# Kernel optimization log

Hardware: AMD Instinct MI355X
Metric: run time of the kernel (lower is better)

The kernel has to match this reference:

```python
import jax, jax.numpy as jnp
import numpy as np

MUL = 64      # multiplicity of each irrep (64x0e + 64x1o)
B = 8192      # batch / number of nodes
INV_SQRT3 = float(1.0 / np.sqrt(3.0))  # e3nn wigner_3j normalization for (1,1,0),(0,1,1),(1,0,1)
# component normalization: alpha = sqrt(dim_out / fan_in), fan_in = sum over paths of mul_u*mul_v
FAN_IN = 2 * MUL * MUL  # two paths feed each output irrep
ALPHA0 = float(np.sqrt(1.0 / FAN_IN))  # l_out = 0, dim 1
ALPHA1 = float(np.sqrt(3.0 / FAN_IN))  # l_out = 1, dim 3


def setup_inputs() -> dict:
    key = jax.random.key(0)
    kx, k0, k1, k2, k3 = jax.random.split(key, 5)
    x = jax.random.normal(kx, (B, 4 * MUL), dtype=jnp.float32)  # [B, 64*1 + 64*3]
    w000 = jax.random.normal(k0, (MUL, MUL, MUL), dtype=jnp.float32)  # 0e x 0e -> 0e
    w110 = jax.random.normal(k1, (MUL, MUL, MUL), dtype=jnp.float32)  # 1o x 1o -> 0e
    w011 = jax.random.normal(k2, (MUL, MUL, MUL), dtype=jnp.float32)  # 0e x 1o -> 1o
    w101 = jax.random.normal(k3, (MUL, MUL, MUL), dtype=jnp.float32)  # 1o x 0e -> 1o
    return {"x": x, "w000": w000, "w110": w110, "w011": w011, "w101": w101}


def reference(x, w000, w110, w011, w101):
    # split concatenated irrep features: scalars then vectors
    x0 = x[:, :MUL]                          # [B, U]      l=0 (e)
    x1 = x[:, MUL:].reshape(-1, MUL, 3)      # [B, U, 3]   l=1 (o)

    # path (0e,0e)->0e : CG = 1
    p000 = jnp.einsum('uvw,bu,bv->bw', w000, x0, x0)
    # path (1o,1o)->0e : CG[i,j] = delta_ij / sqrt(3)
    p110 = jnp.einsum('uvw,bui,bvi->bw', w110, x1, x1) * INV_SQRT3
    out0 = ALPHA0 * (p000 + p110)            # [B, W]

    # path (0e,1o)->1o : CG[j,k] = delta_jk / sqrt(3)
    p011 = jnp.einsum('uvw,bu,bvk->bwk', w011, x0, x1) * INV_SQRT3
    # path (1o,0e)->1o : CG[i,k] = delta_ik / sqrt(3)
    p101 = jnp.einsum('uvw,buk,bv->bwk', w101, x1, x0) * INV_SQRT3
    out1 = ALPHA1 * (p011 + p101)            # [B, W, 3]

    return jnp.concatenate([out0, out1.reshape(out1.shape[0], MUL * 3)], axis=-1)
```

## Files before the change

kernel.cpp:

```cpp
#include <hip/hip_runtime.h>
#include <hip/hip_bf16.h>
#include <cstdint>

#define BM 32
#define NTHREADS 640
#define WS_TILE 524288
#define SMEM_BYTES (4*64*32*4 + 6*32*64*4)

typedef __bf16 bf16x8_t __attribute__((ext_vector_type(8)));
typedef float f32x4_t __attribute__((ext_vector_type(4)));

__global__ __launch_bounds__(256) void prep_weights(const float* __restrict__ w000,
                                                    const float* __restrict__ w110,
                                                    const float* __restrict__ w011,
                                                    const float* __restrict__ w101,
                                                    char* __restrict__ ws) {
  const float A0  = 0.011048543456039806f;
  const float A0I = A0 * 0.57735026918962576f;
  int t = blockIdx.x * 256 + threadIdx.x;
  int u = t >> 9, f = (t >> 6) & 7, l = t & 63;
  int n = f >> 1, kf = f & 1;
  int w = 16 * n + (l & 15);
  int vbase = 8 * (l >> 4) + 32 * kf;
  bf16x8_t p0, p1, pc;
#pragma unroll
  for (int j = 0; j < 8; ++j) {
    int v = vbase + j;
    float a = w000[u * 4096 + v * 64 + w] * A0;
    float b = w110[u * 4096 + v * 64 + w] * A0I;
    float d = (w011[u * 4096 + v * 64 + w] + w101[v * 4096 + u * 64 + w]) * A0;
    p0[j] = (__bf16)a;
    p1[j] = (__bf16)b;
    pc[j] = (__bf16)d;
  }
  int off = u * 8192 + f * 1024 + l * 16;
  *(bf16x8_t*)(ws + off) = p0;
  *(bf16x8_t*)(ws + WS_TILE + off) = p1;
  *(bf16x8_t*)(ws + 2 * WS_TILE + off) = pc;
}

__global__ __launch_bounds__(NTHREADS, 1) void tp_main(const float* __restrict__ x,
                                                       const char* __restrict__ ws,
                                                       float* __restrict__ out) {
  extern __shared__ char smem[];
  float* xS   = (float*)smem;
  float* pscr = (float*)(smem + 32768);
  const int tid = threadIdx.x;
  const int wave = tid >> 6, lane = tid & 63;
  const int lr = lane & 15, lg = lane >> 4;
  const int b0 = blockIdx.x * BM;
  const int unit = wave >> 1;
  const int kf = wave & 1;
  const int tsel = (unit == 0) ? 0 : ((unit == 1) ? 1 : 2);
  const char* gw = ws + tsel * WS_TILE + kf * 1024 + lane * 16;

  for (int idx = tid; idx < 4 * 64 * 32; idx += NTHREADS) {
    int vec = idx >> 11, rem = idx & 2047;
    int uu = rem >> 5, bb = rem & 31;
    int col = (vec == 0) ? uu : (64 + 3 * uu + (vec - 1));
    xS[idx] = x[(b0 + bb) * 256 + col];
  }

  float xp[3][2][8];
  if (unit == 1) {
#pragma unroll
    for (int vi = 0; vi < 3; ++vi)
#pragma unroll
      for (int m = 0; m < 2; ++m)
#pragma unroll
        for (int j = 0; j < 8; ++j) {
          int v = 8 * lg + 32 * kf + j;
          xp[vi][m][j] = x[(b0 + 16 * m + lr) * 256 + 64 + 3 * v + vi];
        }
  } else {
#pragma unroll
    for (int m = 0; m < 2; ++m)
#pragma unroll
      for (int j = 0; j < 8; ++j) {
        int v = 8 * lg + 32 * kf + j;
        int col = (unit == 0) ? v : (64 + 3 * v + (unit - 2));
        xp[0][m][j] = x[(b0 + 16 * m + lr) * 256 + col];
      }
  }

  f32x4_t acc[2][4];
#pragma unroll
  for (int m = 0; m < 2; ++m)
#pragma unroll
    for (int n = 0; n < 4; ++n) {
      f32x4_t z = {0.f, 0.f, 0.f, 0.f};
      acc[m][n] = z;
    }

  auto LOADG = [&](bf16x8_t (&bfr)[4], int uu) {
    const char* p = gw + uu * 8192;
#pragma unroll
    for (int n = 0; n < 4; ++n)
      bfr[n] = *(const bf16x8_t*)(p + n * 2048);
  };

  auto STEP = [&](bf16x8_t (&bfr)[4], int uu) {
    bf16x8_t afr[2];
    if (unit == 1) {
#pragma unroll
      for (int m = 0; m < 2; ++m) {
        float s0 = xS[1 * 2048 + uu * 32 + 16 * m + lr];
        float s1 = xS[2 * 2048 + uu * 32 + 16 * m + lr];
        float s2 = xS[3 * 2048 + uu * 32 + 16 * m + lr];
#pragma unroll
        for (int j = 0; j < 8; ++j)
          afr[m][j] = (__bf16)(s0 * xp[0][m][j] + s1 * xp[1][m][j] + s2 * xp[2][m][j]);
      }
    } else {
#pragma unroll
      for (int m = 0; m < 2; ++m) {
        float s = xS[uu * 32 + 16 * m + lr];
#pragma unroll
        for (int j = 0; j < 8; ++j)
          afr[m][j] = (__bf16)(s * xp[0][m][j]);
      }
    }
#pragma unroll
    for (int m = 0; m < 2; ++m)
#pragma unroll
      for (int n = 0; n < 4; ++n)
        acc[m][n] = __builtin_amdgcn_mfma_f32_16x16x32_bf16(afr[m], bfr[n], acc[m][n], 0, 0, 0);
  };

  __syncthreads();

  bf16x8_t B0[4], B1[4], B2[4];
  LOADG(B0, 0);
  LOADG(B1, 1);
  for (int u = 0; u < 60; u += 3) {
    LOADG(B2, u + 2);
    STEP(B0, u);
    LOADG(B0, u + 3);
    STEP(B1, u + 1);
    LOADG(B1, u + 4);
    STEP(B2, u + 2);
  }
  LOADG(B2, 62);
  STEP(B0, 60);
  LOADG(B0, 63);
  STEP(B1, 61);
  STEP(B2, 62);
  STEP(B0, 63);

  if (kf == 1) {
#pragma unroll
    for (int m = 0; m < 2; ++m)
#pragma unroll
      for (int n = 0; n < 4; ++n)
#pragma unroll
        for (int r = 0; r < 4; ++r)
          pscr[unit * 2048 + (16 * m + 4 * lg + r) * 64 + 16 * n + lr] = acc[m][n][r];
  }
  __syncthreads();
  if (kf == 0) {
#pragma unroll
    for (int m = 0; m < 2; ++m)
#pragma unroll
      for (int n = 0; n < 4; ++n)
#pragma unroll
        for (int r = 0; r < 4; ++r)
          acc[m][n][r] += pscr[unit * 2048 + (16 * m + 4 * lg + r) * 64 + 16 * n + lr];
    if (unit == 1) {
#pragma unroll
      for (int m = 0; m < 2; ++m)
#pragma unroll
        for (int n = 0; n < 4; ++n)
#pragma unroll
          for (int r = 0; r < 4; ++r)
            pscr[5 * 2048 + (16 * m + 4 * lg + r) * 64 + 16 * n + lr] = acc[m][n][r];
    }
  }
  __syncthreads();
  if (wave == 0) {
#pragma unroll
    for (int m = 0; m < 2; ++m)
#pragma unroll
      for (int n = 0; n < 4; ++n)
#pragma unroll
        for (int r = 0; r < 4; ++r) {
          int row = 16 * m + 4 * lg + r, col = 16 * n + lr;
          out[(b0 + row) * 256 + col] = acc[m][n][r] + pscr[5 * 2048 + row * 64 + col];
        }
  } else if (kf == 0 && unit >= 2) {
    const int k = unit - 2;
#pragma unroll
    for (int m = 0; m < 2; ++m)
#pragma unroll
      for (int n = 0; n < 4; ++n)
#pragma unroll
        for (int r = 0; r < 4; ++r) {
          int row = 16 * m + 4 * lg + r, col = 16 * n + lr;
          out[(b0 + row) * 256 + 64 + 3 * col + k] = acc[m][n][r];
        }
  }
}

extern "C" void kernel_launch(void* const* d_in, const int* in_sizes, int n_in,
                              void* d_out, int out_size, void* d_ws, size_t ws_size,
                              hipStream_t stream) {
  const float* x    = (const float*)d_in[0];
  const float* w000 = (const float*)d_in[1];
  const float* w110 = (const float*)d_in[2];
  const float* w011 = (const float*)d_in[3];
  const float* w101 = (const float*)d_in[4];
  float* out = (float*)d_out;
  char* ws = (char*)d_ws;

  prep_weights<<<128, 256, 0, stream>>>(w000, w110, w011, w101, ws);

  hipFuncSetAttribute((const void*)tp_main, hipFuncAttributeMaxDynamicSharedMemorySize, SMEM_BYTES);
  tp_main<<<256, NTHREADS, SMEM_BYTES, stream>>>(x, ws, out);
}
```

Before: 50.53 us.

## Stage weight fragments through LDS with async global_load_lds triple buffering

Weight fragments are now streamed from global memory into per-wave LDS ring buffers with global_load_lds, replacing direct register loads. vmcnt waits pace a three-deep pipeline, and fragments are read back from LDS just before each MFMA step. The intent is to cut register pressure and hide global latency, with launch bounds relaxed so more than one block can share a CU. The cost is an extra LDS round trip per step, and the hand-written vmcnt counts must track exactly which loads are still in flight.

```diff
diff --git a/kernel.cpp b/kernel.cpp
--- a/kernel.cpp
+++ b/kernel.cpp
@@ -5,10 +5,22 @@
 #define BM 32
 #define NTHREADS 640
 #define WS_TILE 524288
-#define SMEM_BYTES (4*64*32*4 + 6*32*64*4)
+#define WAVE_BUF 4096
+#define NBUF 3
+#define STAGE_BYTES (10 * NBUF * WAVE_BUF)
+#define SMEM_BYTES (STAGE_BYTES + 4 * 64 * 32 * 4)
 
 typedef __bf16 bf16x8_t __attribute__((ext_vector_type(8)));
 typedef float f32x4_t __attribute__((ext_vector_type(4)));
+
+__device__ __forceinline__ void async_ld16(const void* g, void* l) {
+  __builtin_amdgcn_global_load_lds((const __attribute__((address_space(1))) unsigned int*)g,
+                                   (__attribute__((address_space(3))) unsigned int*)l,
+                                   16, 0, 0);
+}
+
+#define WAIT4() asm volatile("s_waitcnt vmcnt(4)" ::: "memory")
+#define WAIT0() asm volatile("s_waitcnt vmcnt(0)" ::: "memory")
 
 __global__ __launch_bounds__(256) void prep_weights(const float* __restrict__ w000,
                                                     const float* __restrict__ w110,
@@ -39,12 +51,12 @@
   *(bf16x8_t*)(ws + 2 * WS_TILE + off) = pc;
 }
 
-__global__ __launch_bounds__(NTHREADS, 1) void tp_main(const float* __restrict__ x,
-                                                       const char* __restrict__ ws,
-                                                       float* __restrict__ out) {
+__global__ __launch_bounds__(NTHREADS) void tp_main(const float* __restrict__ x,
+                                                    const char* __restrict__ ws,
+                                                    float* __restrict__ out) {
   extern __shared__ char smem[];
-  float* xS   = (float*)smem;
-  float* pscr = (float*)(smem + 32768);
+  float* xS   = (float*)(smem + STAGE_BYTES);
+  float* pscr = (float*)smem;
   const int tid = threadIdx.x;
   const int wave = tid >> 6, lane = tid & 63;
   const int lr = lane & 15, lg = lane >> 4;
@@ -53,6 +65,22 @@
   const int kf = wave & 1;
   const int tsel = (unit == 0) ? 0 : ((unit == 1) ? 1 : 2);
   const char* gw = ws + tsel * WS_TILE + kf * 1024 + lane * 16;
+  char* myb = smem + wave * (NBUF * WAVE_BUF);
+
+  auto STAGE = [&](int uu, int bsel) {
+    const char* g = gw + uu * 8192;
+    char* l = myb + bsel * WAVE_BUF + lane * 16;
+#pragma unroll
+    for (int n = 0; n < 4; ++n)
+      async_ld16(g + n * 2048, l + n * 1024);
+  };
+
+  auto LOADB = [&](bf16x8_t (&bfr)[4], int bsel) {
+    const char* p = myb + bsel * WAVE_BUF + lane * 16;
+#pragma unroll
+    for (int n = 0; n < 4; ++n)
+      bfr[n] = *(const bf16x8_t*)(p + n * 1024);
+  };
 
   for (int idx = tid; idx < 4 * 64 * 32; idx += NTHREADS) {
     int vec = idx >> 11, rem = idx & 2047;
@@ -92,13 +120,6 @@
       acc[m][n] = z;
     }
 
-  auto LOADG = [&](bf16x8_t (&bfr)[4], int uu) {
-    const char* p = gw + uu * 8192;
-#pragma unroll
-    for (int n = 0; n < 4; ++n)
-      bfr[n] = *(const bf16x8_t*)(p + n * 2048);
-  };
-
   auto STEP = [&](bf16x8_t (&bfr)[4], int uu) {
     bf16x8_t afr[2];
     if (unit == 1) {
@@ -129,24 +150,21 @@
 
   __syncthreads();
 
-  bf16x8_t B0[4], B1[4], B2[4];
-  LOADG(B0, 0);
-  LOADG(B1, 1);
+  STAGE(0, 0);
+  STAGE(1, 1);
+
+  bf16x8_t bfr[4];
   for (int u = 0; u < 60; u += 3) {
-    LOADG(B2, u + 2);
-    STEP(B0, u);
-    LOADG(B0, u + 3);
-    STEP(B1, u + 1);
-    LOADG(B1, u + 4);
-    STEP(B2, u + 2);
-  }
-  LOADG(B2, 62);
-  STEP(B0, 60);
-  LOADG(B0, 63);
-  STEP(B1, 61);
-  STEP(B2, 62);
-  STEP(B0, 63);
-
+    WAIT4(); LOADB(bfr, 0); STAGE(u + 2, 2); STEP(bfr, u);
+    WAIT4(); LOADB(bfr, 1); STAGE(u + 3, 0); STEP(bfr, u + 1);
+    WAIT4(); LOADB(bfr, 2); STAGE(u + 4, 1); STEP(bfr, u + 2);
+  }
+  WAIT4(); LOADB(bfr, 0); STAGE(62, 2); STEP(bfr, 60);
+  WAIT4(); LOADB(bfr, 1); STAGE(63, 0); STEP(bfr, 61);
+  WAIT4(); LOADB(bfr, 2); STEP(bfr, 62);
+  WAIT0(); LOADB(bfr, 0); STEP(bfr, 63);
+
+  __syncthreads();
   if (kf == 1) {
 #pragma unroll
     for (int m = 0; m < 2; ++m)
```

Measured after the change: 52.26 us. +3.4%, slower.
